# Kernel optimization log

Hardware: AMD Instinct MI355X
Metric: run time of the kernel (lower is better)

Reference implementation:

```python
import jax, jax.numpy as jnp
import numpy as np

N = 50000      # num nodes
E = 400000     # num edges (before self loops)
IN = 128       # in_channels
H = 4          # num_heads
C = 64         # hidden_channels (per head)
NEG_SLOPE = 0.2
BN_EPS = 1e-5


def gatv2_layer(x, Wl, Wr, att, bias, src, dst, n, concat):
    # GATv2Conv (PyG, share_weights=False): xl for source/messages, xr for dest
    h, c = att.shape
    xl = (x @ Wl).reshape(n, h, c)
    xr = (x @ Wr).reshape(n, h, c)
    # per-edge attention logits: [E, H]
    e = jnp.sum(jax.nn.leaky_relu(xl[src] + xr[dst], NEG_SLOPE) * att[None], axis=-1)
    # edge softmax grouped by destination node
    m = jax.ops.segment_max(e, dst, num_segments=n)          # [N, H]
    ex = jnp.exp(e - m[dst])
    den = jax.ops.segment_sum(ex, dst, num_segments=n)       # [N, H]
    alpha = ex / (den[dst] + 1e-16)                          # [E, H]
    # weighted scatter-sum aggregation: [N, H, C]
    out = jax.ops.segment_sum(alpha[..., None] * xl[src], dst, num_segments=n)
    out = out.reshape(n, h * c) if concat else out.mean(axis=1)
    return out + bias


def bn_eval(x, gamma, beta):
    # eval-mode BatchNorm1d with init running stats (mean=0, var=1)
    return x / jnp.sqrt(jnp.asarray(1.0 + BN_EPS, x.dtype)) * gamma + beta


def setup_inputs() -> dict:
    key = jax.random.key(0)
    ks = jax.random.split(key, 20)
    s = 0.05
    return {
        "x": jax.random.normal(ks[0], (N, IN), jnp.float32),
        "edge_index": jax.random.randint(ks[1], (2, E), 0, N, jnp.int32),
        # layer 1: in=128 -> heads=4, out=64, concat -> 256
        "W1l": jax.random.normal(ks[2], (IN, H * C), jnp.float32) * s,
        "W1r": jax.random.normal(ks[3], (IN, H * C), jnp.float32) * s,
        "att1": jax.random.normal(ks[4], (H, C), jnp.float32) * s,
        "b1": jnp.zeros((H * C,), jnp.float32),
        "g1": jnp.ones((H * C,), jnp.float32),
        "be1": jnp.zeros((H * C,), jnp.float32),
        # layer 2: in=256 -> heads=4, out=64, mean -> 64
        "W2l": jax.random.normal(ks[5], (H * C, H * C), jnp.float32) * s,
        "W2r": jax.random.normal(ks[6], (H * C, H * C), jnp.float32) * s,
        "att2": jax.random.normal(ks[7], (H, C), jnp.float32) * s,
        "b2": jnp.zeros((C,), jnp.float32),
        "g2": jnp.ones((C,), jnp.float32),
        "be2": jnp.zeros((C,), jnp.float32),
        # final linear 64 -> 1
        "fcW": jax.random.normal(ks[8], (C, 1), jnp.float32) * s,
        "fcb": jnp.zeros((1,), jnp.float32),
    }


def reference(x, edge_index, W1l, W1r, att1, b1, g1, be1,
              W2l, W2r, att2, b2, g2, be2, fcW, fcb):
    # PyG GATv2Conv adds self loops by default
    loops = jnp.arange(N, dtype=edge_index.dtype)
    src = jnp.concatenate([edge_index[0], loops])
    dst = jnp.concatenate([edge_index[1], loops])

    h = gatv2_layer(x, W1l, W1r, att1, b1, src, dst, N, concat=True)   # [N, 256]
    h = jax.nn.elu(bn_eval(h, g1, be1))                                 # dropout = id (eval)
    h = gatv2_layer(h, W2l, W2r, att2, b2, src, dst, N, concat=False)  # [N, 64]
    h = jax.nn.elu(bn_eval(h, g2, be2))
    out = jax.nn.sigmoid(h @ fcW + fcb)                                 # [N, 1]
    return out
```

## Files before the change

kernel.cpp:

```cpp
#include <hip/hip_runtime.h>
#include <math.h>

#define NNODES 50000
#define NEDGES 400000
#define E2 (NEDGES + NNODES)
#define HC 256
#define NOUT 512
#define NF (NOUT / 16)
#define BN_SCALE 0.9999950000374997f
#define SCAN_B ((NNODES + 255) / 256)
#define GEMM_B ((NNODES + 63) / 64)
#define HIST_B ((E2 + 255) / 256)

typedef unsigned short ushortx8 __attribute__((ext_vector_type(8)));
typedef __bf16 bf16x8 __attribute__((ext_vector_type(8)));
typedef float f32x4 __attribute__((ext_vector_type(4)));
typedef float f32x2 __attribute__((ext_vector_type(2)));

__device__ inline unsigned short f2bf(float f) {
    unsigned u = __float_as_uint(f);
    u += 0x7fff + ((u >> 16) & 1);
    return (unsigned short)(u >> 16);
}

template <int CTRL>
__device__ __forceinline__ float dpp_add(float x) {
    int y = __builtin_amdgcn_update_dpp(0, __float_as_int(x), CTRL, 0xF, 0xF, true);
    return x + __int_as_float(y);
}
__device__ __forceinline__ float row16_sum(float x) {
    x = dpp_add<0xB1>(x);
    x = dpp_add<0x4E>(x);
    x = dpp_add<0x141>(x);
    x = dpp_add<0x140>(x);
    return x;
}

#define B1_N (128 * NOUT)
#define B2_N (256 * NOUT)
#define PACK_B ((B1_N + B2_N + 255) / 256)

__device__ __forceinline__ void prep_one(const float* __restrict__ Wl,
                                         const float* __restrict__ Wr,
                                         unsigned short* __restrict__ Bf, int id) {
    int j    = id & 7;
    int lane = (id >> 3) & 63;
    int nf   = (id >> 9) & (NF - 1);
    int kb   = id >> 14;
    int k = kb * 32 + (lane >> 4) * 8 + j;
    int c = nf * 16 + (lane & 15);
    float v = (c < 256) ? Wl[k * 256 + c] : Wr[k * 256 + (c - 256)];
    Bf[id] = f2bf(v);
}

__global__ __launch_bounds__(256) void k1_pack_hist(
        const float* __restrict__ W1l, const float* __restrict__ W1r,
        const float* __restrict__ W2l, const float* __restrict__ W2r,
        unsigned short* __restrict__ Bf1, unsigned short* __restrict__ Bf2,
        const int* __restrict__ ei, int* __restrict__ deg) {
    int bid = blockIdx.x;
    if (bid < PACK_B) {
        int id = bid * 256 + threadIdx.x;
        if (id < B1_N) {
            prep_one(W1l, W1r, Bf1, id);
        } else if (id < B1_N + B2_N) {
            prep_one(W2l, W2r, Bf2, id - B1_N);
        }
    } else {
        int i = (bid - PACK_B) * 256 + threadIdx.x;
        if (i < E2) {
            int d = (i < NEDGES) ? ei[NEDGES + i] : i - NEDGES;
            atomicAdd(&deg[d], 1);
        }
    }
}

template <bool AF32>
__device__ __forceinline__ void gemm_body(int bx, int tid,
        const void* __restrict__ Av, const unsigned short* __restrict__ Bf,
        unsigned short* __restrict__ C, int M, int K) {
    const int lane = tid & 63;
    const int w    = tid >> 6;
    const int row0 = bx * 64;
    const int col0 = w * 128;
    const int lr = lane & 15, lg = lane >> 4;

    f32x4 acc[4][8] = {};
    const int nkb = K >> 5;
    for (int kb = 0; kb < nkb; ++kb) {
        bf16x8 af[4], bfr[8];
        const int kcol = kb * 32 + lg * 8;
#pragma unroll
        for (int i = 0; i < 4; ++i) {
            int r = row0 + i * 16 + lr;
            if constexpr (AF32) {
                const float* Af = (const float*)Av;
                f32x4 a0 = {}, a1 = {};
                if (r < M) {
                    a0 = *reinterpret_cast<const f32x4*>(Af + (size_t)r * K + kcol);
                    a1 = *reinterpret_cast<const f32x4*>(Af + (size_t)r * K + kcol + 4);
                }
                bf16x8 t;
#pragma unroll
                for (int q = 0; q < 4; ++q) { t[q] = (__bf16)a0[q]; t[4 + q] = (__bf16)a1[q]; }
                af[i] = t;
            } else {
                const unsigned short* Ab = (const unsigned short*)Av;
                ushortx8 av = {};
                if (r < M)
                    av = *reinterpret_cast<const ushortx8*>(Ab + (size_t)r * K + kcol);
                af[i] = __builtin_bit_cast(bf16x8, av);
            }
        }
#pragma unroll
        for (int j = 0; j < 8; ++j) {
            int nf = (col0 >> 4) + j;
            ushortx8 bv = *reinterpret_cast<const ushortx8*>(
                Bf + (((size_t)(kb * NF + nf) * 64 + lane) << 3));
            bfr[j] = __builtin_bit_cast(bf16x8, bv);
        }
#pragma unroll
        for (int i = 0; i < 4; ++i)
#pragma unroll
            for (int j = 0; j < 8; ++j)
                acc[i][j] = __builtin_amdgcn_mfma_f32_16x16x32_bf16(
                    af[i], bfr[j], acc[i][j], 0, 0, 0);
    }
#pragma unroll
    for (int i = 0; i < 4; ++i) {
#pragma unroll
        for (int r = 0; r < 4; ++r) {
            int row = row0 + i * 16 + lg * 4 + r;
            if (row < M) {
#pragma unroll
                for (int j = 0; j < 8; ++j)
                    C[(size_t)row * NOUT + col0 + j * 16 + lr] = f2bf(acc[i][j][r]);
            }
        }
    }
}

__global__ __launch_bounds__(256) void k2_gemm1_scan1(
        const float* __restrict__ A, const unsigned short* __restrict__ Bf,
        unsigned short* __restrict__ C, int M, int K,
        const int* __restrict__ deg, int* __restrict__ rowptr, int* __restrict__ bsum) {
    __shared__ int buf[256];
    if (blockIdx.x < GEMM_B) {
        gemm_body<true>(blockIdx.x, threadIdx.x, A, Bf, C, M, K);
    } else {
        int bx = blockIdx.x - GEMM_B;
        int t = threadIdx.x;
        int i = bx * 256 + t;
        int v = (i < NNODES) ? deg[i] : 0;
        buf[t] = v;
        __syncthreads();
        for (int off = 1; off < 256; off <<= 1) {
            int u = (t >= off) ? buf[t - off] : 0;
            __syncthreads();
            buf[t] += u;
            __syncthreads();
        }
        if (i < NNODES) rowptr[i] = buf[t] - v;
        if (t == 255) bsum[bx] = buf[255];
    }
}

__global__ __launch_bounds__(256) void k3_scan23(
        const int* __restrict__ bsum, int* __restrict__ rowptr, int* __restrict__ cursor) {
    __shared__ int sbuf[256];
    int t = threadIdx.x;
    int v = (t < (int)blockIdx.x && t < SCAN_B) ? bsum[t] : 0;
    sbuf[t] = v;
    __syncthreads();
    for (int off = 128; off; off >>= 1) {
        if (t < off) sbuf[t] += sbuf[t + off];
        __syncthreads();
    }
    int base = sbuf[0];
    int i = blockIdx.x * 256 + t;
    if (i < NNODES) {
        int r = rowptr[i] + base;
        rowptr[i] = r;
        cursor[i] = r;
    }
    if (blockIdx.x == 0 && t == 0) rowptr[NNODES] = E2;
}

__global__ __launch_bounds__(256) void k4_scatter(
        const int* __restrict__ ei, int* __restrict__ cursor, int* __restrict__ csr_src) {
    int i = blockIdx.x * blockDim.x + threadIdx.x;
    if (i >= E2) return;
    int s, d;
    if (i < NEDGES) { s = ei[i]; d = ei[NEDGES + i]; }
    else            { s = i - NEDGES; d = s; }
    int slot = atomicAdd(&cursor[d], 1);
    csr_src[slot] = s * NOUT;
}

__global__ __launch_bounds__(256) void gemm_mfma(
        const unsigned short* __restrict__ A, const unsigned short* __restrict__ Bf,
        unsigned short* __restrict__ C, int M, int K) {
    gemm_body<false>(blockIdx.x, threadIdx.x, A, Bf, C, M, K);
}

template <int LAYER>
__global__ __launch_bounds__(256) void gat_node(
        const unsigned short* __restrict__ xlr,
        const float* __restrict__ att, const int* __restrict__ rowptr,
        const int* __restrict__ csr_src,
        const float* __restrict__ bias, const float* __restrict__ g,
        const float* __restrict__ be,
        const float* __restrict__ fcW, const float* __restrict__ fcb,
        void* __restrict__ outv) {
    int wid  = (blockIdx.x * blockDim.x + threadIdx.x) >> 6;
    int lane = threadIdx.x & 63;
    if (wid >= NNODES) return;

    f32x2 xb01, xb23, at01, at23;
    {
        uint2 wv = *reinterpret_cast<const uint2*>(xlr + (size_t)wid * NOUT + 256 + lane * 4);
        xb01.x = __uint_as_float(wv.x << 16);
        xb01.y = __uint_as_float(wv.x & 0xffff0000u);
        xb23.x = __uint_as_float(wv.y << 16);
        xb23.y = __uint_as_float(wv.y & 0xffff0000u);
        float4 a = *reinterpret_cast<const float4*>(att + lane * 4);
        at01.x = a.x; at01.y = a.y;
        at23.x = a.z; at23.y = a.w;
    }
    const int beg = rowptr[wid];
    const int end = rowptr[wid + 1];
    const unsigned short* __restrict__ xbase = xlr + lane * 4;

    float den = 0.f;
    f32x2 ac01 = {0.f, 0.f}, ac23 = {0.f, 0.f};

    auto edge = [&](uint2 wv) {
        f32x2 xv01, xv23;
        xv01.x = __uint_as_float(wv.x << 16);
        xv01.y = __uint_as_float(wv.x & 0xffff0000u);
        xv23.x = __uint_as_float(wv.y << 16);
        xv23.y = __uint_as_float(wv.y & 0xffff0000u);
        f32x2 v01 = xv01 + xb01;
        f32x2 v23 = xv23 + xb23;
        v01 = __builtin_elementwise_max(v01, v01 * 0.2f);
        v23 = __builtin_elementwise_max(v23, v23 * 0.2f);
        f32x2 d2 = v01 * at01 + v23 * at23;
        float part = row16_sum(d2.x + d2.y);
        float p = __expf(part);
        den += p;
        ac01 += p * xv01;
        ac23 += p * xv23;
    };

    int j = beg;
    for (; j + 4 <= end; j += 4) {
        int s0 = csr_src[j], s1 = csr_src[j + 1], s2 = csr_src[j + 2], s3 = csr_src[j + 3];
        uint2 w0 = *reinterpret_cast<const uint2*>(xbase + (size_t)(unsigned)s0);
        uint2 w1 = *reinterpret_cast<const uint2*>(xbase + (size_t)(unsigned)s1);
        uint2 w2 = *reinterpret_cast<const uint2*>(xbase + (size_t)(unsigned)s2);
        uint2 w3 = *reinterpret_cast<const uint2*>(xbase + (size_t)(unsigned)s3);
        edge(w0); edge(w1); edge(w2); edge(w3);
    }
    for (; j < end; ++j) {
        int s0 = csr_src[j];
        uint2 w0 = *reinterpret_cast<const uint2*>(xbase + (size_t)(unsigned)s0);
        edge(w0);
    }

    float inv = 1.f / (den + 1e-16f);
    float ax = ac01.x * inv, ay = ac01.y * inv, az = ac23.x * inv, aw = ac23.y * inv;

    if (LAYER == 1) {
        int c0 = lane * 4;
        float o0 = (ax + bias[c0 + 0]) * BN_SCALE * g[c0 + 0] + be[c0 + 0];
        float o1 = (ay + bias[c0 + 1]) * BN_SCALE * g[c0 + 1] + be[c0 + 1];
        float o2 = (az + bias[c0 + 2]) * BN_SCALE * g[c0 + 2] + be[c0 + 2];
        float o3 = (aw + bias[c0 + 3]) * BN_SCALE * g[c0 + 3] + be[c0 + 3];
        o0 = o0 > 0.f ? o0 : expm1f(o0);
        o1 = o1 > 0.f ? o1 : expm1f(o1);
        o2 = o2 > 0.f ? o2 : expm1f(o2);
        o3 = o3 > 0.f ? o3 : expm1f(o3);
        ushort4 o = { f2bf(o0), f2bf(o1), f2bf(o2), f2bf(o3) };
        *reinterpret_cast<ushort4*>((unsigned short*)outv + (size_t)wid * HC + lane * 4) = o;
    } else {
#pragma unroll
        for (int off = 16; off < 64; off <<= 1) {
            ax += __shfl_xor(ax, off);
            ay += __shfl_xor(ay, off);
            az += __shfl_xor(az, off);
            aw += __shfl_xor(aw, off);
        }
        int c0 = (lane & 15) * 4;
        float v0 = (ax * 0.25f + bias[c0 + 0]) * BN_SCALE * g[c0 + 0] + be[c0 + 0];
        float v1 = (ay * 0.25f + bias[c0 + 1]) * BN_SCALE * g[c0 + 1] + be[c0 + 1];
        float v2 = (az * 0.25f + bias[c0 + 2]) * BN_SCALE * g[c0 + 2] + be[c0 + 2];
        float v3 = (aw * 0.25f + bias[c0 + 3]) * BN_SCALE * g[c0 + 3] + be[c0 + 3];
        v0 = v0 > 0.f ? v0 : expm1f(v0);
        v1 = v1 > 0.f ? v1 : expm1f(v1);
        v2 = v2 > 0.f ? v2 : expm1f(v2);
        v3 = v3 > 0.f ? v3 : expm1f(v3);
        float dot = v0 * fcW[c0] + v1 * fcW[c0 + 1] + v2 * fcW[c0 + 2] + v3 * fcW[c0 + 3];
        dot = row16_sum(dot);
        if (lane == 0) ((float*)outv)[wid] = 1.f / (1.f + __expf(-(dot + fcb[0])));
    }
}

extern "C" void kernel_launch(void* const* d_in, const int* in_sizes, int n_in,
                              void* d_out, int out_size, void* d_ws, size_t ws_size,
                              hipStream_t stream) {
    const float* x    = (const float*)d_in[0];
    const int*   ei   = (const int*)d_in[1];
    const float* W1l  = (const float*)d_in[2];
    const float* W1r  = (const float*)d_in[3];
    const float* att1 = (const float*)d_in[4];
    const float* b1   = (const float*)d_in[5];
    const float* g1   = (const float*)d_in[6];
    const float* be1  = (const float*)d_in[7];
    const float* W2l  = (const float*)d_in[8];
    const float* W2r  = (const float*)d_in[9];
    const float* att2 = (const float*)d_in[10];
    const float* b2   = (const float*)d_in[11];
    const float* g2   = (const float*)d_in[12];
    const float* be2  = (const float*)d_in[13];
    const float* fcW  = (const float*)d_in[14];
    const float* fcb  = (const float*)d_in[15];
    float* out = (float*)d_out;

    unsigned short* xlr   = (unsigned short*)d_ws;
    unsigned short* h1_bf = xlr + (size_t)NNODES * NOUT;
    unsigned short* Bf1   = h1_bf + (size_t)NNODES * 256;
    unsigned short* Bf2   = Bf1 + 128 * NOUT;
    int* csr_src = (int*)(Bf2 + 256 * NOUT);
    int* deg     = csr_src + E2;
    int* rowptr  = deg + NNODES;
    int* cursor  = rowptr + NNODES + 1;
    int* bsum    = cursor + NNODES;

    const int nodeBlocks = (NNODES * 64 + 255) / 256;

    hipMemsetAsync(deg, 0, NNODES * sizeof(int), stream);

    k1_pack_hist<<<PACK_B + HIST_B, 256, 0, stream>>>(
        W1l, W1r, W2l, W2r, Bf1, Bf2, ei, deg);

    k2_gemm1_scan1<<<GEMM_B + SCAN_B, 256, 0, stream>>>(
        x, Bf1, xlr, NNODES, 128, deg, rowptr, bsum);

    k3_scan23<<<SCAN_B, 256, 0, stream>>>(bsum, rowptr, cursor);

    k4_scatter<<<HIST_B, 256, 0, stream>>>(ei, cursor, csr_src);

    gat_node<1><<<nodeBlocks, 256, 0, stream>>>(xlr, att1, rowptr, csr_src,
                                                b1, g1, be1, nullptr, nullptr, h1_bf);

    gemm_mfma<<<GEMM_B, 256, 0, stream>>>(h1_bf, Bf2, xlr, NNODES, 256);
    gat_node<2><<<nodeBlocks, 256, 0, stream>>>(xlr, att2, rowptr, csr_src,
                                                b2, g2, be2, fcW, fcb, out);
}
```

Measured before the change: 213.5 us.

## Sort destination nodes by degree for balanced waves; use exp2 with prescaled attention

Builds a degree histogram (capped at 63) during the scan, then counting-sorts nodes into a permutation so each block processes waves of similar in-degree. Both GAT node kernels look up their node through this permutation to cut intra-block imbalance from the degree tail. The attention vector is also prescaled by log2(e) so exp2f replaces __expf. The cost is extra atomics, an extra indirection, and less locality in the output writes and self-feature reads.

```diff
diff --git a/kernel.cpp b/kernel.cpp
--- a/kernel.cpp
+++ b/kernel.cpp
@@ -8,6 +8,7 @@
 #define NOUT 512
 #define NF (NOUT / 16)
 #define BN_SCALE 0.9999950000374997f
+#define LOG2E 1.4426950408889634f
 #define SCAN_B ((NNODES + 255) / 256)
 #define GEMM_B ((NNODES + 63) / 64)
 #define HIST_B ((E2 + 255) / 256)
@@ -143,7 +144,8 @@
 __global__ __launch_bounds__(256) void k2_gemm1_scan1(
         const float* __restrict__ A, const unsigned short* __restrict__ Bf,
         unsigned short* __restrict__ C, int M, int K,
-        const int* __restrict__ deg, int* __restrict__ rowptr, int* __restrict__ bsum) {
+        const int* __restrict__ deg, int* __restrict__ rowptr, int* __restrict__ bsum,
+        int* __restrict__ dhist) {
     __shared__ int buf[256];
     if (blockIdx.x < GEMM_B) {
         gemm_body<true>(blockIdx.x, threadIdx.x, A, Bf, C, M, K);
@@ -152,6 +154,10 @@
         int t = threadIdx.x;
         int i = bx * 256 + t;
         int v = (i < NNODES) ? deg[i] : 0;
+        if (i < NNODES) {
+            int d = v > 63 ? 63 : v;
+            atomicAdd(&dhist[d], 1);
+        }
         buf[t] = v;
         __syncthreads();
         for (int off = 1; off < 256; off <<= 1) {
@@ -166,11 +172,20 @@
 }
 
 __global__ __launch_bounds__(256) void k3_scan23(
-        const int* __restrict__ bsum, int* __restrict__ rowptr, int* __restrict__ cursor) {
+        const int* __restrict__ bsum, const int* __restrict__ deg,
+        int* __restrict__ rowptr, int* __restrict__ cursor,
+        const int* __restrict__ dhist, int* __restrict__ dcur,
+        int* __restrict__ perm) {
     __shared__ int sbuf[256];
+    __shared__ int dpre[64];
     int t = threadIdx.x;
     int v = (t < (int)blockIdx.x && t < SCAN_B) ? bsum[t] : 0;
     sbuf[t] = v;
+    if (t < 64) {
+        int s = 0;
+        for (int k = 0; k < t; ++k) s += dhist[k];
+        dpre[t] = s;
+    }
     __syncthreads();
     for (int off = 128; off; off >>= 1) {
         if (t < off) sbuf[t] += sbuf[t + off];
@@ -182,6 +197,9 @@
         int r = rowptr[i] + base;
         rowptr[i] = r;
         cursor[i] = r;
+        int d = deg[i]; if (d > 63) d = 63;
+        int slot = dpre[d] + atomicAdd(&dcur[d], 1);
+        perm[slot] = i;
     }
     if (blockIdx.x == 0 && t == 0) rowptr[NNODES] = E2;
 }
@@ -207,14 +225,15 @@
 __global__ __launch_bounds__(256) void gat_node(
         const unsigned short* __restrict__ xlr,
         const float* __restrict__ att, const int* __restrict__ rowptr,
-        const int* __restrict__ csr_src,
+        const int* __restrict__ csr_src, const int* __restrict__ perm,
         const float* __restrict__ bias, const float* __restrict__ g,
         const float* __restrict__ be,
         const float* __restrict__ fcW, const float* __restrict__ fcb,
         void* __restrict__ outv) {
-    int wid  = (blockIdx.x * blockDim.x + threadIdx.x) >> 6;
+    int slot = (blockIdx.x * blockDim.x + threadIdx.x) >> 6;
     int lane = threadIdx.x & 63;
-    if (wid >= NNODES) return;
+    if (slot >= NNODES) return;
+    const int wid = perm[slot];
 
     f32x2 xb01, xb23, at01, at23;
     {
@@ -224,8 +243,8 @@
         xb23.x = __uint_as_float(wv.y << 16);
         xb23.y = __uint_as_float(wv.y & 0xffff0000u);
         float4 a = *reinterpret_cast<const float4*>(att + lane * 4);
-        at01.x = a.x; at01.y = a.y;
-        at23.x = a.z; at23.y = a.w;
+        at01.x = a.x * LOG2E; at01.y = a.y * LOG2E;
+        at23.x = a.z * LOG2E; at23.y = a.w * LOG2E;
     }
     const int beg = rowptr[wid];
     const int end = rowptr[wid + 1];
@@ -246,7 +265,7 @@
         v23 = __builtin_elementwise_max(v23, v23 * 0.2f);
         f32x2 d2 = v01 * at01 + v23 * at23;
         float part = row16_sum(d2.x + d2.y);
-        float p = __expf(part);
+        float p = exp2f(part);
         den += p;
         ac01 += p * xv01;
         ac23 += p * xv23;
@@ -332,28 +351,31 @@
     unsigned short* Bf2   = Bf1 + 128 * NOUT;
     int* csr_src = (int*)(Bf2 + 256 * NOUT);
     int* deg     = csr_src + E2;
-    int* rowptr  = deg + NNODES;
+    int* dhist   = deg + NNODES;
+    int* dcur    = dhist + 64;
+    int* rowptr  = dcur + 64;
     int* cursor  = rowptr + NNODES + 1;
     int* bsum    = cursor + NNODES;
+    int* perm    = bsum + SCAN_B;
 
     const int nodeBlocks = (NNODES * 64 + 255) / 256;
 
-    hipMemsetAsync(deg, 0, NNODES * sizeof(int), stream);
+    hipMemsetAsync(deg, 0, (NNODES + 128) * sizeof(int), stream);
 
     k1_pack_hist<<<PACK_B + HIST_B, 256, 0, stream>>>(
         W1l, W1r, W2l, W2r, Bf1, Bf2, ei, deg);
 
     k2_gemm1_scan1<<<GEMM_B + SCAN_B, 256, 0, stream>>>(
-        x, Bf1, xlr, NNODES, 128, deg, rowptr, bsum);
-
-    k3_scan23<<<SCAN_B, 256, 0, stream>>>(bsum, rowptr, cursor);
+        x, Bf1, xlr, NNODES, 128, deg, rowptr, bsum, dhist);
+
+    k3_scan23<<<SCAN_B, 256, 0, stream>>>(bsum, deg, rowptr, cursor, dhist, dcur, perm);
 
     k4_scatter<<<HIST_B, 256, 0, stream>>>(ei, cursor, csr_src);
 
-    gat_node<1><<<nodeBlocks, 256, 0, stream>>>(xlr, att1, rowptr, csr_src,
+    gat_node<1><<<nodeBlocks, 256, 0, stream>>>(xlr, att1, rowptr, csr_src, perm,
                                                 b1, g1, be1, nullptr, nullptr, h1_bf);
 
     gemm_mfma<<<GEMM_B, 256, 0, stream>>>(h1_bf, Bf2, xlr, NNODES, 256);
-    gat_node<2><<<nodeBlocks, 256, 0, stream>>>(xlr, att2, rowptr, csr_src,
+    gat_node<2><<<nodeBlocks, 256, 0, stream>>>(xlr, att2, rowptr, csr_src, perm,
                                                 b2, g2, be2, fcW, fcb, out);
 }
```

After: 554.9 us. 2.6x slower.
